# Kernel optimization log

Measured on AMD Instinct MI355X. Metric: run time of the kernel, lower is better.

The kernel has to match this reference:

```python
import jax, jax.numpy as jnp
import numpy as np

B, S, T, IN, H = 16384, 336, 48, 5, 64  # batch, enc seq, horizon, features, hidden


def _lstm_cell(x, h, c, Wih, Whh, bih, bhh):
    # PyTorch gate order: i, f, g, o
    g = x @ Wih.T + h @ Whh.T + bih + bhh  # [B, 4H]
    i, f, gg, o = jnp.split(g, 4, axis=-1)
    i, f, o = jax.nn.sigmoid(i), jax.nn.sigmoid(f), jax.nn.sigmoid(o)
    c_new = f * c + i * jnp.tanh(gg)
    h_new = o * jnp.tanh(c_new)
    return h_new, c_new


def setup_inputs() -> dict:
    key = jax.random.key(0)
    ks = jax.random.split(key, 20)
    k = 1.0 / np.sqrt(H)

    def p(kk, shape):
        return jax.random.uniform(kk, shape, jnp.float32, -k, k)

    d = {"src": jax.random.normal(ks[0], (B, S, IN), jnp.float32)}
    d["enc_Wih0"] = p(ks[1], (4 * H, IN)); d["enc_Whh0"] = p(ks[2], (4 * H, H))
    d["enc_bih0"] = p(ks[3], (4 * H,));   d["enc_bhh0"] = p(ks[4], (4 * H,))
    d["enc_Wih1"] = p(ks[5], (4 * H, H)); d["enc_Whh1"] = p(ks[6], (4 * H, H))
    d["enc_bih1"] = p(ks[7], (4 * H,));   d["enc_bhh1"] = p(ks[8], (4 * H,))
    d["dec_Wih0"] = p(ks[9], (4 * H, 1)); d["dec_Whh0"] = p(ks[10], (4 * H, H))
    d["dec_bih0"] = p(ks[11], (4 * H,));  d["dec_bhh0"] = p(ks[12], (4 * H,))
    d["dec_Wih1"] = p(ks[13], (4 * H, H)); d["dec_Whh1"] = p(ks[14], (4 * H, H))
    d["dec_bih1"] = p(ks[15], (4 * H,));  d["dec_bhh1"] = p(ks[16], (4 * H,))
    d["fc_W"] = p(ks[17], (1, H)); d["fc_b"] = p(ks[18], (1,))
    return d


def reference(src, enc_Wih0, enc_Whh0, enc_bih0, enc_bhh0,
              enc_Wih1, enc_Whh1, enc_bih1, enc_bhh1,
              dec_Wih0, dec_Whh0, dec_bih0, dec_bhh0,
              dec_Wih1, dec_Whh1, dec_bih1, dec_bhh1,
              fc_W, fc_b):
    b = src.shape[0]
    z = jnp.zeros((b, H), src.dtype)

    # ---- Encoder: 2-layer LSTM over S timesteps (inference: no dropout) ----
    def enc_step(carry, x_t):
        h0, c0, h1, c1 = carry
        h0, c0 = _lstm_cell(x_t, h0, c0, enc_Wih0, enc_Whh0, enc_bih0, enc_bhh0)
        h1, c1 = _lstm_cell(h0, h1, c1, enc_Wih1, enc_Whh1, enc_bih1, enc_bhh1)
        return (h0, c0, h1, c1), None

    (h0, c0, h1, c1), _ = jax.lax.scan(enc_step, (z, z, z, z),
                                       jnp.swapaxes(src, 0, 1))  # [S,B,IN]

    dec_in0 = src[:, -1, 3:4]  # [B, 1] (feature index 3 of last timestep)

    def dec_step(carry, _):
        h0, c0, h1, c1, x = carry
        h0, c0 = _lstm_cell(x, h0, c0, dec_Wih0, dec_Whh0, dec_bih0, dec_bhh0)
        h1, c1 = _lstm_cell(h0, h1, c1, dec_Wih1, dec_Whh1, dec_bih1, dec_bhh1)
        pred = h1 @ fc_W.T + fc_b  # [B, 1]
        return (h0, c0, h1, c1, pred), pred

    _, preds = jax.lax.scan(dec_step, (h0, c0, h1, c1, dec_in0), None, length=T)
    return jnp.transpose(preds, (1, 0, 2))  # [B, T, 1]
```

## Files before the change

### kernel.cpp

```cpp
#include <hip/hip_runtime.h>
#include <stdint.h>

#define B_ 16384
#define S_ 336
#define T_ 48
#define IN_ 5
#define H_ 64

#define ROWS 32
#define NT   (ROWS / 16)
#define GP   (ROWS * 8)

typedef _Float16 f16;
typedef _Float16 f16x8 __attribute__((ext_vector_type(8)));
typedef float f32x4 __attribute__((ext_vector_type(4)));

#define LOG2E 1.44269504088896340736f

#define OFF_E0 0
#define OFF_E1 24576
#define OFF_D0 57344
#define OFF_D1 81920
#define OFF_BE0 114688
#define OFF_BE1 114944
#define OFF_BD0 115200
#define OFF_BD1 115456
#define OFF_FCW 115712
#define OFF_FCB 115776
#define WS_TOT  115777

__device__ __forceinline__ float sig2(float g) {
    return __builtin_amdgcn_rcpf(1.0f + __builtin_amdgcn_exp2f(g));
}
__device__ __forceinline__ float tanh2(float g) {
    return 1.0f - 2.0f * __builtin_amdgcn_rcpf(1.0f + __builtin_amdgcn_exp2f(g));
}
__device__ __forceinline__ float tanhc(float c) {
    return 1.0f - 2.0f * __builtin_amdgcn_rcpf(1.0f + __builtin_amdgcn_exp2f(c * (2.0f * LOG2E)));
}

__global__ void prep_kernel(
    const float* __restrict__ eWih0, const float* __restrict__ eWhh0,
    const float* __restrict__ ebih0, const float* __restrict__ ebhh0,
    const float* __restrict__ eWih1, const float* __restrict__ eWhh1,
    const float* __restrict__ ebih1, const float* __restrict__ ebhh1,
    const float* __restrict__ dWih0, const float* __restrict__ dWhh0,
    const float* __restrict__ dbih0, const float* __restrict__ dbhh0,
    const float* __restrict__ dWih1, const float* __restrict__ dWhh1,
    const float* __restrict__ dbih1, const float* __restrict__ dbhh1,
    const float* __restrict__ fcW,  const float* __restrict__ fcb,
    float* __restrict__ ws)
{
    int idx = blockIdx.x * blockDim.x + threadIdx.x;
    if (idx >= WS_TOT) return;
    float outv;
    if (idx < OFF_BE0) {
        int rel, nkt, xdim;
        const float *Wi, *Wh, *bi, *bh;
        if (idx < OFF_E1)      { rel = idx - OFF_E0; nkt = 3; xdim = IN_; Wi = eWih0; Wh = eWhh0; bi = ebih0; bh = ebhh0; }
        else if (idx < OFF_D0) { rel = idx - OFF_E1; nkt = 4; xdim = 64;  Wi = eWih1; Wh = eWhh1; bi = 0; bh = 0; }
        else if (idx < OFF_D1) { rel = idx - OFF_D0; nkt = 3; xdim = 1;   Wi = dWih0; Wh = dWhh0; bi = dbih0; bh = dbhh0; }
        else                   { rel = idx - OFF_D1; nkt = 4; xdim = 64;  Wi = dWih1; Wh = dWhh1; bi = 0; bh = 0; }
        int reg = rel & 3, pl = (rel >> 2) & 1, lane = (rel >> 3) & 63;
        int rest = rel >> 9;
        int kt = rest % nkt, mt = rest / nkt;
        int gp = mt * 16 + (lane & 15);
        int type = gp & 3;
        int j  = type * 64 + (gp >> 2);
        float sc = (type == 2) ? (2.0f * LOG2E) : (-LOG2E);
        union { f16 h2[2]; float f; } u_;
        #pragma unroll
        for (int h = 0; h < 2; ++h) {
            int k = kt * 32 + (lane >> 4) * 8 + reg * 2 + h;
            float v;
            if (nkt == 4)      v = (k < 64) ? Wi[j * 64 + k] : Wh[j * 64 + (k - 64)];
            else if (k < xdim) v = Wi[j * xdim + k];
            else if (k == 5)   v = bi[j] + bh[j];
            else if (k >= 32)  v = Wh[j * 64 + (k - 32)];
            else               v = 0.0f;
            v *= sc;
            f16 hi = (f16)v;
            u_.h2[h] = (pl == 0) ? hi : (f16)(v - (float)hi);
        }
        outv = u_.f;
    } else if (idx < OFF_FCW) {
        int rel = idx - OFF_BE0;
        int which = rel >> 8, gp = rel & 255;
        int type = gp & 3;
        int j = type * 64 + (gp >> 2);
        float sc = (type == 2) ? (2.0f * LOG2E) : (-LOG2E);
        const float *bi, *bh;
        if (which == 0)      { bi = ebih0; bh = ebhh0; }
        else if (which == 1) { bi = ebih1; bh = ebhh1; }
        else if (which == 2) { bi = dbih0; bh = dbhh0; }
        else                 { bi = dbih1; bh = dbhh1; }
        outv = (bi[j] + bh[j]) * sc;
    } else if (idx < OFF_FCB) {
        outv = fcW[idx - OFF_FCW];
    } else {
        outv = fcb[0];
    }
    ws[idx] = outv;
}

#define XBI(b,p,g,r)   ((((b)*2+(p))*4+(g))*GP + (r)*8)
#define HBI(b,p,k,g,r) (((((b)*2+(p))*2+(k))*4+(g))*GP + (r)*8)
#define XTOT (2*2*4*GP)
#define HHALF (2*2*4*GP)

#define MFMA(a,b,c) __builtin_amdgcn_mfma_f32_16x16x32_f16(a, b, c, 0, 0, 0)

__device__ __forceinline__ void stage_x5(f16* __restrict__ XB, int b, int r, const float* xv) {
    f16x8 ph, pl_;
    #pragma unroll
    for (int i = 0; i < 8; ++i) { ph[i] = (f16)0; pl_[i] = (f16)0; }
    #pragma unroll
    for (int i = 0; i < IN_; ++i) {
        f16 hh = (f16)xv[i]; ph[i] = hh; pl_[i] = (f16)(xv[i] - (float)hh);
    }
    ph[5] = (f16)1.0f;
    *(f16x8*)&XB[XBI(b,0,0,r)] = ph;
    *(f16x8*)&XB[XBI(b,1,0,r)] = pl_;
}
__device__ __forceinline__ void stage_x1(f16* __restrict__ XB, int b, int r, float v) {
    f16x8 ph, pl_;
    #pragma unroll
    for (int i = 0; i < 8; ++i) { ph[i] = (f16)0; pl_[i] = (f16)0; }
    f16 hh = (f16)v; ph[0] = hh; pl_[0] = (f16)(v - (float)hh);
    ph[5] = (f16)1.0f;
    *(f16x8*)&XB[XBI(b,0,0,r)] = ph;
    *(f16x8*)&XB[XBI(b,1,0,r)] = pl_;
}

__device__ __forceinline__ void layer0_only(
    int pX, int pH0r, int pH0w, int m0, int lane,
    const f16x8 (&wa)[7][2], float (&c0)[2][NT],
    const f16* __restrict__ XB, f16* __restrict__ H0B)
{
    const int g4 = lane >> 4, l15 = lane & 15;
    #pragma unroll
    for (int nt = 0; nt < NT; ++nt) {
        const int r = nt * 16 + l15;
        f16x8 xh  = *(const f16x8*)&XB [XBI(pX,0,g4,r)];
        f16x8 xl  = *(const f16x8*)&XB [XBI(pX,1,g4,r)];
        f16x8 hh0 = *(const f16x8*)&H0B[HBI(pH0r,0,0,g4,r)];
        f16x8 hl0 = *(const f16x8*)&H0B[HBI(pH0r,1,0,g4,r)];
        f16x8 hh1 = *(const f16x8*)&H0B[HBI(pH0r,0,1,g4,r)];
        f16x8 hl1 = *(const f16x8*)&H0B[HBI(pH0r,1,1,g4,r)];
        #pragma unroll
        for (int mt = 0; mt < 2; ++mt) {
            f32x4 z = {0.0f, 0.0f, 0.0f, 0.0f};
            z = MFMA(wa[0][mt], xh,  z);
            z = MFMA(wa[0][mt], xl,  z);
            z = MFMA(wa[1][mt], hh0, z);
            z = MFMA(wa[1][mt], hl0, z);
            z = MFMA(wa[2][mt], hh1, z);
            z = MFMA(wa[2][mt], hl1, z);
            const int u = (m0 + mt) * 4 + g4;
            float ig = sig2(z[0]), fg = sig2(z[1]);
            float gg = tanh2(z[2]), og = sig2(z[3]);
            float c = fmaf(fg, c0[mt][nt], ig * gg);
            c0[mt][nt] = c;
            float h = og * tanhc(c);
            f16 hh = (f16)h, hl = (f16)(h - (float)hh);
            H0B[HBI(pH0w,0,(u>>5),(u>>3)&3,r) + (u&7)] = hh;
            H0B[HBI(pH0w,1,(u>>5),(u>>3)&3,r) + (u&7)] = hl;
        }
    }
}

template<bool DEC>
__device__ __forceinline__ void layer1_only(
    int pH0, int pH1r, int pH1w, int m0, int lane,
    const f16x8 (&wa)[7][2], const f32x4 (&b1)[2], float (&c1)[2][NT],
    const f16* __restrict__ H0B, f16* __restrict__ H1B, float* __restrict__ H1F)
{
    const int g4 = lane >> 4, l15 = lane & 15;
    #pragma unroll
    for (int nt = 0; nt < NT; ++nt) {
        const int r = nt * 16 + l15;
        f16x8 hh0 = *(const f16x8*)&H0B[HBI(pH0,0,0,g4,r)];
        f16x8 hl0 = *(const f16x8*)&H0B[HBI(pH0,1,0,g4,r)];
        f16x8 hh1 = *(const f16x8*)&H0B[HBI(pH0,0,1,g4,r)];
        f16x8 hl1 = *(const f16x8*)&H0B[HBI(pH0,1,1,g4,r)];
        f16x8 gh0 = *(const f16x8*)&H1B[HBI(pH1r,0,0,g4,r)];
        f16x8 gl0 = *(const f16x8*)&H1B[HBI(pH1r,1,0,g4,r)];
        f16x8 gh1 = *(const f16x8*)&H1B[HBI(pH1r,0,1,g4,r)];
        f16x8 gl1 = *(const f16x8*)&H1B[HBI(pH1r,1,1,g4,r)];
        #pragma unroll
        for (int mt = 0; mt < 2; ++mt) {
            f32x4 a = b1[mt];
            a = MFMA(wa[3][mt], hh0, a);
            a = MFMA(wa[3][mt], hl0, a);
            a = MFMA(wa[4][mt], hh1, a);
            a = MFMA(wa[4][mt], hl1, a);
            a = MFMA(wa[5][mt], gh0, a);
            a = MFMA(wa[5][mt], gl0, a);
            a = MFMA(wa[6][mt], gh1, a);
            a = MFMA(wa[6][mt], gl1, a);
            const int u = (m0 + mt) * 4 + g4;
            float ig = sig2(a[0]), fg = sig2(a[1]);
            float gg = tanh2(a[2]), og = sig2(a[3]);
            float c = fmaf(fg, c1[mt][nt], ig * gg);
            c1[mt][nt] = c;
            float h = og * tanhc(c);
            f16 hh = (f16)h, hl = (f16)(h - (float)hh);
            H1B[HBI(pH1w,0,(u>>5),(u>>3)&3,r) + (u&7)] = hh;
            H1B[HBI(pH1w,1,(u>>5),(u>>3)&3,r) + (u&7)] = hl;
            if (DEC) H1F[u * 33 + r] = h;
        }
    }
}

__device__ __forceinline__ void enc_phase(
    int p, int m0, int lane,
    const f16x8 (&wa)[7][2], const f32x4 (&b1)[2],
    float (&c0)[2][NT], float (&c1)[2][NT],
    const f16* __restrict__ XB, f16* __restrict__ H0B, f16* __restrict__ H1B)
{
    const int g4 = lane >> 4, l15 = lane & 15;
    const int q = p ^ 1;
    #pragma unroll
    for (int nt = 0; nt < NT; ++nt) {
        const int r = nt * 16 + l15;
        f16x8 hh0 = *(const f16x8*)&H0B[HBI(p,0,0,g4,r)];
        f16x8 hl0 = *(const f16x8*)&H0B[HBI(p,1,0,g4,r)];
        f16x8 hh1 = *(const f16x8*)&H0B[HBI(p,0,1,g4,r)];
        f16x8 hl1 = *(const f16x8*)&H0B[HBI(p,1,1,g4,r)];
        f16x8 gh0 = *(const f16x8*)&H1B[HBI(q,0,0,g4,r)];
        f16x8 gl0 = *(const f16x8*)&H1B[HBI(q,1,0,g4,r)];
        f16x8 gh1 = *(const f16x8*)&H1B[HBI(q,0,1,g4,r)];
        f16x8 gl1 = *(const f16x8*)&H1B[HBI(q,1,1,g4,r)];
        #pragma unroll
        for (int mt = 0; mt < 2; ++mt) {
            const int u = (m0 + mt) * 4 + g4;
            f32x4 a = b1[mt];
            a = MFMA(wa[3][mt], hh0, a);
            a = MFMA(wa[3][mt], hl0, a);
            a = MFMA(wa[4][mt], hh1, a);
            a = MFMA(wa[4][mt], hl1, a);
            a = MFMA(wa[5][mt], gh0, a);
            a = MFMA(wa[5][mt], gl0, a);
            a = MFMA(wa[6][mt], gh1, a);
            a = MFMA(wa[6][mt], gl1, a);
            float ig = sig2(a[0]), fg = sig2(a[1]);
            float gg = tanh2(a[2]), og = sig2(a[3]);
            float c = fmaf(fg, c1[mt][nt], ig * gg);
            c1[mt][nt] = c;
            float h = og * tanhc(c);
            f16 hh = (f16)h, hl = (f16)(h - (float)hh);
            H1B[HBI(p,0,(u>>5),(u>>3)&3,r) + (u&7)] = hh;
            H1B[HBI(p,1,(u>>5),(u>>3)&3,r) + (u&7)] = hl;
        }
        f16x8 xh = *(const f16x8*)&XB[XBI(q,0,g4,r)];
        f16x8 xl = *(const f16x8*)&XB[XBI(q,1,g4,r)];
        #pragma unroll
        for (int mt = 0; mt < 2; ++mt) {
            const int u = (m0 + mt) * 4 + g4;
            f32x4 z = {0.0f, 0.0f, 0.0f, 0.0f};
            z = MFMA(wa[0][mt], xh,  z);
            z = MFMA(wa[0][mt], xl,  z);
            z = MFMA(wa[1][mt], hh0, z);
            z = MFMA(wa[1][mt], hl0, z);
            z = MFMA(wa[2][mt], hh1, z);
            z = MFMA(wa[2][mt], hl1, z);
            float ig = sig2(z[0]), fg = sig2(z[1]);
            float gg = tanh2(z[2]), og = sig2(z[3]);
            float c = fmaf(fg, c0[mt][nt], ig * gg);
            c0[mt][nt] = c;
            float h = og * tanhc(c);
            f16 hh = (f16)h, hl = (f16)(h - (float)hh);
            H0B[HBI(q,0,(u>>5),(u>>3)&3,r) + (u&7)] = hh;
            H0B[HBI(q,1,(u>>5),(u>>3)&3,r) + (u&7)] = hl;
        }
    }
}

__global__ __launch_bounds__(512) void lstm_kernel(
    const float* __restrict__ src, const float* __restrict__ ws,
    float* __restrict__ out)
{
    __shared__ __align__(16) f16 XB [XTOT];
    __shared__ __align__(16) f16 H0B[2*HHALF];
    __shared__ __align__(16) f16 H1B[2*HHALF];
    __shared__ float H1F[64*33];
    __shared__ float FCW[64];

    const int tid  = threadIdx.x;
    const int lane = tid & 63;
    const int wave = __builtin_amdgcn_readfirstlane(tid >> 6);
    const int m0   = wave * 2;
    const int g4   = lane >> 4;
    const int rowBase = blockIdx.x * ROWS;

    float c0[2][NT], c1[2][NT];
    #pragma unroll
    for (int mt = 0; mt < 2; ++mt)
        #pragma unroll
        for (int nt = 0; nt < NT; ++nt) { c0[mt][nt] = 0.0f; c1[mt][nt] = 0.0f; }

    f16x8 wa[7][2];
    f32x4 b1[2];

    auto ldw = [&](int off0, int off1, int ob1) {
        #pragma unroll
        for (int kt = 0; kt < 3; ++kt)
            #pragma unroll
            for (int mt = 0; mt < 2; ++mt)
                wa[kt][mt] = *(const f16x8*)(ws + off0 +
                    ((((m0 + mt) * 3 + kt) * 64 + lane) * 2) * 4);
        #pragma unroll
        for (int kt = 0; kt < 4; ++kt)
            #pragma unroll
            for (int mt = 0; mt < 2; ++mt)
                wa[3 + kt][mt] = *(const f16x8*)(ws + off1 +
                    ((((m0 + mt) * 4 + kt) * 64 + lane) * 2) * 4);
        #pragma unroll
        for (int mt = 0; mt < 2; ++mt)
            b1[mt] = *(const f32x4*)(ws + ob1 + (m0 + mt) * 16 + g4 * 4);
    };
    ldw(OFF_E0, OFF_E1, OFF_BE1);

    for (int i = tid; i < XTOT; i += 512) XB[i] = (f16)0;
    for (int i = tid; i < HHALF; i += 512) { H0B[HHALF + i] = (f16)0; H1B[HHALF + i] = (f16)0; }
    if (tid < 64) FCW[tid] = ws[OFF_FCW + tid];
    const float fcbv = ws[OFF_FCB];

    const int xr = lane & (ROWS - 1);
    const float* sp = src + (size_t)(rowBase + xr) * (S_ * IN_);
    __syncthreads();

    if (wave == 7 && lane < ROWS) {
        float xv[IN_];
        #pragma unroll
        for (int i = 0; i < IN_; ++i) xv[i] = sp[i];
        stage_x5(XB, 0, lane, xv);
        #pragma unroll
        for (int i = 0; i < IN_; ++i) xv[i] = sp[IN_ + i];
        stage_x5(XB, 1, lane, xv);
    }
    __syncthreads();

    layer0_only(0, 1, 0, m0, lane, wa, c0, XB, H0B);
    __syncthreads();

    #pragma unroll 1
    for (int t = 0; t < S_ - 1; ++t) {
        const int p = t & 1;
        float xv[IN_];
        const bool pf = (wave == 7) && (lane < ROWS) && (t + 2 < S_);
        if (pf) {
            #pragma unroll
            for (int i = 0; i < IN_; ++i) xv[i] = sp[(t + 2) * IN_ + i];
        }
        enc_phase(p, m0, lane, wa, b1, c0, c1, XB, H0B, H1B);
        if (pf) stage_x5(XB, p, lane, xv);
        __syncthreads();
    }

    layer1_only<false>(1, 0, 1, m0, lane, wa, b1, c1, H0B, H1B, H1F);
    __syncthreads();

    ldw(OFF_D0, OFF_D1, OFF_BD1);
    if (wave == 7 && lane < ROWS) stage_x1(XB, 0, lane, sp[(S_ - 1) * IN_ + 3]);
    __syncthreads();

    #pragma unroll 1
    for (int t = 0; t < T_; ++t) {
        const int q = t & 1;
        layer0_only(q, q ^ 1, q, m0, lane, wa, c0, XB, H0B);
        __syncthreads();
        layer1_only<true>(q, q ^ 1, q, m0, lane, wa, b1, c1, H0B, H1B, H1F);
        __syncthreads();
        if (wave == 0 && lane < ROWS) {
            float pv = fcbv;
            #pragma unroll 4
            for (int k = 0; k < 64; ++k) pv = fmaf(FCW[k], H1F[k * 33 + lane], pv);
            out[(size_t)(rowBase + lane) * T_ + t] = pv;
            if (t + 1 < T_) stage_x1(XB, q ^ 1, lane, pv);
        }
        __syncthreads();
    }
}

extern "C" void kernel_launch(void* const* d_in, const int* in_sizes, int n_in,
                              void* d_out, int out_size, void* d_ws, size_t ws_size,
                              hipStream_t stream)
{
    const float* src = (const float*)d_in[0];
    float* ws  = (float*)d_ws;
    float* out = (float*)d_out;

    prep_kernel<<<(WS_TOT + 255) / 256, 256, 0, stream>>>(
        (const float*)d_in[1],  (const float*)d_in[2],
        (const float*)d_in[3],  (const float*)d_in[4],
        (const float*)d_in[5],  (const float*)d_in[6],
        (const float*)d_in[7],  (const float*)d_in[8],
        (const float*)d_in[9],  (const float*)d_in[10],
        (const float*)d_in[11], (const float*)d_in[12],
        (const float*)d_in[13], (const float*)d_in[14],
        (const float*)d_in[15], (const float*)d_in[16],
        (const float*)d_in[17], (const float*)d_in[18],
        ws);

    lstm_kernel<<<B_ / ROWS, 512, 0, stream>>>(src, ws, out);
}
```

Before: 1.745 ms.

## Split gate M-tiles across 16 waves and interleave both layers' MFMA chains

```diff
diff --git a/kernel.cpp b/kernel.cpp
--- a/kernel.cpp
+++ b/kernel.cpp
@@ -133,11 +133,12 @@
 }
 
 __device__ __forceinline__ void layer0_only(
-    int pX, int pH0r, int pH0w, int m0, int lane,
-    const f16x8 (&wa)[7][2], float (&c0)[2][NT],
+    int pX, int pH0r, int pH0w, int wave, int lane,
+    const f16x8 (&wa)[7], float (&c0)[NT],
     const f16* __restrict__ XB, f16* __restrict__ H0B)
 {
     const int g4 = lane >> 4, l15 = lane & 15;
+    const int u = wave * 4 + g4;
     #pragma unroll
     for (int nt = 0; nt < NT; ++nt) {
         const int r = nt * 16 + l15;
@@ -147,35 +148,32 @@
         f16x8 hl0 = *(const f16x8*)&H0B[HBI(pH0r,1,0,g4,r)];
         f16x8 hh1 = *(const f16x8*)&H0B[HBI(pH0r,0,1,g4,r)];
         f16x8 hl1 = *(const f16x8*)&H0B[HBI(pH0r,1,1,g4,r)];
-        #pragma unroll
-        for (int mt = 0; mt < 2; ++mt) {
-            f32x4 z = {0.0f, 0.0f, 0.0f, 0.0f};
-            z = MFMA(wa[0][mt], xh,  z);
-            z = MFMA(wa[0][mt], xl,  z);
-            z = MFMA(wa[1][mt], hh0, z);
-            z = MFMA(wa[1][mt], hl0, z);
-            z = MFMA(wa[2][mt], hh1, z);
-            z = MFMA(wa[2][mt], hl1, z);
-            const int u = (m0 + mt) * 4 + g4;
-            float ig = sig2(z[0]), fg = sig2(z[1]);
-            float gg = tanh2(z[2]), og = sig2(z[3]);
-            float c = fmaf(fg, c0[mt][nt], ig * gg);
-            c0[mt][nt] = c;
-            float h = og * tanhc(c);
-            f16 hh = (f16)h, hl = (f16)(h - (float)hh);
-            H0B[HBI(pH0w,0,(u>>5),(u>>3)&3,r) + (u&7)] = hh;
-            H0B[HBI(pH0w,1,(u>>5),(u>>3)&3,r) + (u&7)] = hl;
-        }
+        f32x4 z = {0.0f, 0.0f, 0.0f, 0.0f};
+        z = MFMA(wa[0], xh,  z);
+        z = MFMA(wa[0], xl,  z);
+        z = MFMA(wa[1], hh0, z);
+        z = MFMA(wa[1], hl0, z);
+        z = MFMA(wa[2], hh1, z);
+        z = MFMA(wa[2], hl1, z);
+        float ig = sig2(z[0]), fg = sig2(z[1]);
+        float gg = tanh2(z[2]), og = sig2(z[3]);
+        float c = fmaf(fg, c0[nt], ig * gg);
+        c0[nt] = c;
+        float h = og * tanhc(c);
+        f16 hh = (f16)h, hl = (f16)(h - (float)hh);
+        H0B[HBI(pH0w,0,(u>>5),(u>>3)&3,r) + (u&7)] = hh;
+        H0B[HBI(pH0w,1,(u>>5),(u>>3)&3,r) + (u&7)] = hl;
     }
 }
 
 template<bool DEC>
 __device__ __forceinline__ void layer1_only(
-    int pH0, int pH1r, int pH1w, int m0, int lane,
-    const f16x8 (&wa)[7][2], const f32x4 (&b1)[2], float (&c1)[2][NT],
+    int pH0, int pH1r, int pH1w, int wave, int lane,
+    const f16x8 (&wa)[7], const f32x4 b1, float (&c1)[NT],
     const f16* __restrict__ H0B, f16* __restrict__ H1B, float* __restrict__ H1F)
 {
     const int g4 = lane >> 4, l15 = lane & 15;
+    const int u = wave * 4 + g4;
     #pragma unroll
     for (int nt = 0; nt < NT; ++nt) {
         const int r = nt * 16 + l15;
@@ -187,39 +185,36 @@
         f16x8 gl0 = *(const f16x8*)&H1B[HBI(pH1r,1,0,g4,r)];
         f16x8 gh1 = *(const f16x8*)&H1B[HBI(pH1r,0,1,g4,r)];
         f16x8 gl1 = *(const f16x8*)&H1B[HBI(pH1r,1,1,g4,r)];
-        #pragma unroll
-        for (int mt = 0; mt < 2; ++mt) {
-            f32x4 a = b1[mt];
-            a = MFMA(wa[3][mt], hh0, a);
-            a = MFMA(wa[3][mt], hl0, a);
-            a = MFMA(wa[4][mt], hh1, a);
-            a = MFMA(wa[4][mt], hl1, a);
-            a = MFMA(wa[5][mt], gh0, a);
-            a = MFMA(wa[5][mt], gl0, a);
-            a = MFMA(wa[6][mt], gh1, a);
-            a = MFMA(wa[6][mt], gl1, a);
-            const int u = (m0 + mt) * 4 + g4;
-            float ig = sig2(a[0]), fg = sig2(a[1]);
-            float gg = tanh2(a[2]), og = sig2(a[3]);
-            float c = fmaf(fg, c1[mt][nt], ig * gg);
-            c1[mt][nt] = c;
-            float h = og * tanhc(c);
-            f16 hh = (f16)h, hl = (f16)(h - (float)hh);
-            H1B[HBI(pH1w,0,(u>>5),(u>>3)&3,r) + (u&7)] = hh;
-            H1B[HBI(pH1w,1,(u>>5),(u>>3)&3,r) + (u&7)] = hl;
-            if (DEC) H1F[u * 33 + r] = h;
-        }
+        f32x4 a = b1;
+        a = MFMA(wa[3], hh0, a);
+        a = MFMA(wa[3], hl0, a);
+        a = MFMA(wa[4], hh1, a);
+        a = MFMA(wa[4], hl1, a);
+        a = MFMA(wa[5], gh0, a);
+        a = MFMA(wa[5], gl0, a);
+        a = MFMA(wa[6], gh1, a);
+        a = MFMA(wa[6], gl1, a);
+        float ig = sig2(a[0]), fg = sig2(a[1]);
+        float gg = tanh2(a[2]), og = sig2(a[3]);
+        float c = fmaf(fg, c1[nt], ig * gg);
+        c1[nt] = c;
+        float h = og * tanhc(c);
+        f16 hh = (f16)h, hl = (f16)(h - (float)hh);
+        H1B[HBI(pH1w,0,(u>>5),(u>>3)&3,r) + (u&7)] = hh;
+        H1B[HBI(pH1w,1,(u>>5),(u>>3)&3,r) + (u&7)] = hl;
+        if (DEC) H1F[u * 33 + r] = h;
     }
 }
 
 __device__ __forceinline__ void enc_phase(
-    int p, int m0, int lane,
-    const f16x8 (&wa)[7][2], const f32x4 (&b1)[2],
-    float (&c0)[2][NT], float (&c1)[2][NT],
+    int p, int wave, int lane,
+    const f16x8 (&wa)[7], const f32x4 b1,
+    float (&c0)[NT], float (&c1)[NT],
     const f16* __restrict__ XB, f16* __restrict__ H0B, f16* __restrict__ H1B)
 {
     const int g4 = lane >> 4, l15 = lane & 15;
     const int q = p ^ 1;
+    const int u = wave * 4 + g4;
     #pragma unroll
     for (int nt = 0; nt < NT; ++nt) {
         const int r = nt * 16 + l15;
@@ -231,52 +226,36 @@
         f16x8 gl0 = *(const f16x8*)&H1B[HBI(q,1,0,g4,r)];
         f16x8 gh1 = *(const f16x8*)&H1B[HBI(q,0,1,g4,r)];
         f16x8 gl1 = *(const f16x8*)&H1B[HBI(q,1,1,g4,r)];
-        #pragma unroll
-        for (int mt = 0; mt < 2; ++mt) {
-            const int u = (m0 + mt) * 4 + g4;
-            f32x4 a = b1[mt];
-            a = MFMA(wa[3][mt], hh0, a);
-            a = MFMA(wa[3][mt], hl0, a);
-            a = MFMA(wa[4][mt], hh1, a);
-            a = MFMA(wa[4][mt], hl1, a);
-            a = MFMA(wa[5][mt], gh0, a);
-            a = MFMA(wa[5][mt], gl0, a);
-            a = MFMA(wa[6][mt], gh1, a);
-            a = MFMA(wa[6][mt], gl1, a);
-            float ig = sig2(a[0]), fg = sig2(a[1]);
-            float gg = tanh2(a[2]), og = sig2(a[3]);
-            float c = fmaf(fg, c1[mt][nt], ig * gg);
-            c1[mt][nt] = c;
-            float h = og * tanhc(c);
-            f16 hh = (f16)h, hl = (f16)(h - (float)hh);
-            H1B[HBI(p,0,(u>>5),(u>>3)&3,r) + (u&7)] = hh;
-            H1B[HBI(p,1,(u>>5),(u>>3)&3,r) + (u&7)] = hl;
-        }
-        f16x8 xh = *(const f16x8*)&XB[XBI(q,0,g4,r)];
-        f16x8 xl = *(const f16x8*)&XB[XBI(q,1,g4,r)];
-        #pragma unroll
-        for (int mt = 0; mt < 2; ++mt) {
-            const int u = (m0 + mt) * 4 + g4;
-            f32x4 z = {0.0f, 0.0f, 0.0f, 0.0f};
-            z = MFMA(wa[0][mt], xh,  z);
-            z = MFMA(wa[0][mt], xl,  z);
-            z = MFMA(wa[1][mt], hh0, z);
-            z = MFMA(wa[1][mt], hl0, z);
-            z = MFMA(wa[2][mt], hh1, z);
-            z = MFMA(wa[2][mt], hl1, z);
-            float ig = sig2(z[0]), fg = sig2(z[1]);
-            float gg = tanh2(z[2]), og = sig2(z[3]);
-            float c = fmaf(fg, c0[mt][nt], ig * gg);
-            c0[mt][nt] = c;
-            float h = og * tanhc(c);
-            f16 hh = (f16)h, hl = (f16)(h - (float)hh);
-            H0B[HBI(q,0,(u>>5),(u>>3)&3,r) + (u&7)] = hh;
-            H0B[HBI(q,1,(u>>5),(u>>3)&3,r) + (u&7)] = hl;
-        }
-    }
-}
-
-__global__ __launch_bounds__(512) void lstm_kernel(
+        f16x8 xh  = *(const f16x8*)&XB [XBI(q,0,g4,r)];
+        f16x8 xl  = *(const f16x8*)&XB [XBI(q,1,g4,r)];
+        f32x4 a = b1;
+        f32x4 z = {0.0f, 0.0f, 0.0f, 0.0f};
+        a = MFMA(wa[3], hh0, a);  z = MFMA(wa[0], xh,  z);
+        a = MFMA(wa[3], hl0, a);  z = MFMA(wa[0], xl,  z);
+        a = MFMA(wa[4], hh1, a);  z = MFMA(wa[1], hh0, z);
+        a = MFMA(wa[4], hl1, a);  z = MFMA(wa[1], hl0, z);
+        a = MFMA(wa[5], gh0, a);  z = MFMA(wa[2], hh1, z);
+        a = MFMA(wa[5], gl0, a);  z = MFMA(wa[2], hl1, z);
+        a = MFMA(wa[6], gh1, a);
+        a = MFMA(wa[6], gl1, a);
+        float ia = sig2(a[0]), iz = sig2(z[0]);
+        float fa = sig2(a[1]), fz = sig2(z[1]);
+        float ga = tanh2(a[2]), gz = tanh2(z[2]);
+        float oa = sig2(a[3]), oz = sig2(z[3]);
+        float ca = fmaf(fa, c1[nt], ia * ga); c1[nt] = ca;
+        float cz = fmaf(fz, c0[nt], iz * gz); c0[nt] = cz;
+        float ha = oa * tanhc(ca);
+        float hz = oz * tanhc(cz);
+        f16 hah = (f16)ha, hal = (f16)(ha - (float)hah);
+        f16 hzh = (f16)hz, hzl = (f16)(hz - (float)hzh);
+        H1B[HBI(p,0,(u>>5),(u>>3)&3,r) + (u&7)] = hah;
+        H1B[HBI(p,1,(u>>5),(u>>3)&3,r) + (u&7)] = hal;
+        H0B[HBI(q,0,(u>>5),(u>>3)&3,r) + (u&7)] = hzh;
+        H0B[HBI(q,1,(u>>5),(u>>3)&3,r) + (u&7)] = hzl;
+    }
+}
+
+__global__ __launch_bounds__(1024) void lstm_kernel(
     const float* __restrict__ src, const float* __restrict__ ws,
     float* __restrict__ out)
 {
@@ -289,40 +268,29 @@
     const int tid  = threadIdx.x;
     const int lane = tid & 63;
     const int wave = __builtin_amdgcn_readfirstlane(tid >> 6);
-    const int m0   = wave * 2;
     const int g4   = lane >> 4;
     const int rowBase = blockIdx.x * ROWS;
 
-    float c0[2][NT], c1[2][NT];
-    #pragma unroll
-    for (int mt = 0; mt < 2; ++mt)
-        #pragma unroll
-        for (int nt = 0; nt < NT; ++nt) { c0[mt][nt] = 0.0f; c1[mt][nt] = 0.0f; }
-
-    f16x8 wa[7][2];
-    f32x4 b1[2];
+    float c0[NT], c1[NT];
+    #pragma unroll
+    for (int nt = 0; nt < NT; ++nt) { c0[nt] = 0.0f; c1[nt] = 0.0f; }
+
+    f16x8 wa[7];
+    f32x4 b1;
 
     auto ldw = [&](int off0, int off1, int ob1) {
         #pragma unroll
         for (int kt = 0; kt < 3; ++kt)
-            #pragma unroll
-            for (int mt = 0; mt < 2; ++mt)
-                wa[kt][mt] = *(const f16x8*)(ws + off0 +
-                    ((((m0 + mt) * 3 + kt) * 64 + lane) * 2) * 4);
+            wa[kt] = *(const f16x8*)(ws + off0 + ((wave * 3 + kt) * 64 + lane) * 8);
         #pragma unroll
         for (int kt = 0; kt < 4; ++kt)
-            #pragma unroll
-            for (int mt = 0; mt < 2; ++mt)
-                wa[3 + kt][mt] = *(const f16x8*)(ws + off1 +
-                    ((((m0 + mt) * 4 + kt) * 64 + lane) * 2) * 4);
-        #pragma unroll
-        for (int mt = 0; mt < 2; ++mt)
-            b1[mt] = *(const f32x4*)(ws + ob1 + (m0 + mt) * 16 + g4 * 4);
+            wa[3 + kt] = *(const f16x8*)(ws + off1 + ((wave * 4 + kt) * 64 + lane) * 8);
+        b1 = *(const f32x4*)(ws + ob1 + wave * 16 + g4 * 4);
     };
     ldw(OFF_E0, OFF_E1, OFF_BE1);
 
-    for (int i = tid; i < XTOT; i += 512) XB[i] = (f16)0;
-    for (int i = tid; i < HHALF; i += 512) { H0B[HHALF + i] = (f16)0; H1B[HHALF + i] = (f16)0; }
+    for (int i = tid; i < XTOT; i += 1024) XB[i] = (f16)0;
+    for (int i = tid; i < HHALF; i += 1024) { H0B[HHALF + i] = (f16)0; H1B[HHALF + i] = (f16)0; }
     if (tid < 64) FCW[tid] = ws[OFF_FCW + tid];
     const float fcbv = ws[OFF_FCB];
 
@@ -330,7 +298,7 @@
     const float* sp = src + (size_t)(rowBase + xr) * (S_ * IN_);
     __syncthreads();
 
-    if (wave == 7 && lane < ROWS) {
+    if (wave == 15 && lane < ROWS) {
         float xv[IN_];
         #pragma unroll
         for (int i = 0; i < IN_; ++i) xv[i] = sp[i];
@@ -341,36 +309,36 @@
     }
     __syncthreads();
 
-    layer0_only(0, 1, 0, m0, lane, wa, c0, XB, H0B);
+    layer0_only(0, 1, 0, wave, lane, wa, c0, XB, H0B);
     __syncthreads();
 
     #pragma unroll 1
     for (int t = 0; t < S_ - 1; ++t) {
         const int p = t & 1;
         float xv[IN_];
-        const bool pf = (wave == 7) && (lane < ROWS) && (t + 2 < S_);
+        const bool pf = (wave == 15) && (lane < ROWS) && (t + 2 < S_);
         if (pf) {
             #pragma unroll
             for (int i = 0; i < IN_; ++i) xv[i] = sp[(t + 2) * IN_ + i];
         }
-        enc_phase(p, m0, lane, wa, b1, c0, c1, XB, H0B, H1B);
+        enc_phase(p, wave, lane, wa, b1, c0, c1, XB, H0B, H1B);
         if (pf) stage_x5(XB, p, lane, xv);
         __syncthreads();
     }
 
-    layer1_only<false>(1, 0, 1, m0, lane, wa, b1, c1, H0B, H1B, H1F);
+    layer1_only<false>(1, 0, 1, wave, lane, wa, b1, c1, H0B, H1B, H1F);
     __syncthreads();
 
     ldw(OFF_D0, OFF_D1, OFF_BD1);
-    if (wave == 7 && lane < ROWS) stage_x1(XB, 0, lane, sp[(S_ - 1) * IN_ + 3]);
+    if (wave == 15 && lane < ROWS) stage_x1(XB, 0, lane, sp[(S_ - 1) * IN_ + 3]);
     __syncthreads();
 
     #pragma unroll 1
     for (int t = 0; t < T_; ++t) {
         const int q = t & 1;
-        layer0_only(q, q ^ 1, q, m0, lane, wa, c0, XB, H0B);
+        layer0_only(q, q ^ 1, q, wave, lane, wa, c0, XB, H0B);
         __syncthreads();
-        layer1_only<true>(q, q ^ 1, q, m0, lane, wa, b1, c1, H0B, H1B, H1F);
+        layer1_only<true>(q, q ^ 1, q, wave, lane, wa, b1, c1, H0B, H1B, H1F);
         __syncthreads();
         if (wave == 0 && lane < ROWS) {
             float pv = fcbv;
@@ -403,5 +371,5 @@
         (const float*)d_in[17], (const float*)d_in[18],
         ws);
 
-    lstm_kernel<<<B_ / ROWS, 512, 0, stream>>>(src, ws, out);
-}
+    lstm_kernel<<<B_ / ROWS, 1024, 0, stream>>>(src, ws, out);
+}
```

Result: faster. 1.685 ms (-3.4%).
